# Kernel optimization log

Hardware: AMD Instinct MI355X
Metric: run time of the kernel (lower is better)

The kernel has to match this reference:

```python
import jax, jax.numpy as jnp
import numpy as np

D = 128  # embedding dim (hardcoded by nn.Linear(128*2, 1))


def setup_inputs() -> dict:
    key = jax.random.key(0)
    k1, k2, k3, k4 = jax.random.split(key, 4)
    B, T, N = 256, 64, 2048
    targetsentence_emb = jax.random.normal(k1, (B, T, D), dtype=jnp.float32)
    context_emb = jax.random.normal(k2, (B, N, D), dtype=jnp.float32)
    # Linear(2D -> 1): weight [1, 2D], bias [1]. Store as flat vectors.
    W = jax.random.normal(k3, (2 * D,), dtype=jnp.float32) * (1.0 / np.sqrt(2 * D))
    b = jax.random.normal(k4, (1,), dtype=jnp.float32) * 0.01
    return {"targetsentence_emb": targetsentence_emb, "context_emb": context_emb, "W": W, "b": b}


def reference(targetsentence_emb, context_emb, W, b):
    # Decompose concat+Linear: W = [Wt | Wc], both length D.
    Wt, Wc = W[:D], W[D:]
    T = targetsentence_emb.shape[1]
    # score[b, n] = sum_t (Wt . target[b,t] + Wc . ctx[b,n] + bias)
    #            = sum_t(Wt . target[b,t]) + T * (Wc . ctx[b,n] + bias)
    tgt_term = jnp.einsum('btd,d->b', targetsentence_emb, Wt)  # [B]
    ctx_term = jnp.einsum('bnd,d->bn', context_emb, Wc)        # [B, N]
    scores = tgt_term[:, None] + T * (ctx_term + b[0])         # [B, N]
    attention = jax.nn.softmax(scores, axis=1)                 # softmax over context dim
    # einsum 'bnm,bnk->bnk' with m=1 is elementwise broadcast scaling
    return attention[:, :, None] * context_emb                 # [B, N, D]
```

## Files before the change

### kernel.cpp

```cpp
#include <hip/hip_runtime.h>


#define B_DIM 256
#define N_DIM 2048
#define D_DIM 128
#define DVEC  (D_DIM / 4)
#define NTHR  1024
#define T_SCALE 64.0f

typedef float f4v __attribute__((ext_vector_type(4)));

__global__ __launch_bounds__(NTHR)
void k_fused(const float* __restrict__ ctx, const float* __restrict__ W,
             float* __restrict__ out) {
    const int tid  = threadIdx.x;
    const int wave = tid >> 6;
    const int lane = tid & 63;
    const int sub  = lane & 31;
    const int half = lane >> 5;
    const int b    = blockIdx.x;

    __shared__ float sm[N_DIM];
    __shared__ float red[16];

    const size_t cbase = (size_t)b * ((size_t)N_DIM * DVEC);
    const f4v* __restrict__ c4 = (const f4v*)ctx + cbase;
    f4v*       __restrict__ o4 = (f4v*)out + cbase;

    const f4v wc = ((const f4v*)(W + D_DIM))[sub];

    #pragma unroll 4
    for (int it = 0; it < N_DIM / 32; ++it) {
        const int n = it * 32 + wave * 2 + half;
        const f4v v = c4[(size_t)n * DVEC + sub];
        float p = v.x * wc.x + v.y * wc.y + v.z * wc.z + v.w * wc.w;
        #pragma unroll
        for (int m = 1; m < 32; m <<= 1) p += __shfl_xor(p, m, 64);
        if (sub == 0) sm[n] = T_SCALE * p;
    }
    __syncthreads();

    const float a0 = sm[tid];
    const float a1 = sm[tid + NTHR];
    float mx = fmaxf(a0, a1);
    #pragma unroll
    for (int m = 1; m < 64; m <<= 1) mx = fmaxf(mx, __shfl_xor(mx, m, 64));
    if (lane == 0) red[wave] = mx;
    __syncthreads();
    float gmax = red[0];
    #pragma unroll
    for (int i = 1; i < 16; ++i) gmax = fmaxf(gmax, red[i]);

    const float e0 = __expf(a0 - gmax);
    const float e1 = __expf(a1 - gmax);
    float s = e0 + e1;
    #pragma unroll
    for (int m = 1; m < 64; m <<= 1) s += __shfl_xor(s, m, 64);
    __syncthreads();
    if (lane == 0) red[wave] = s;
    __syncthreads();
    float tot = red[0];
    #pragma unroll
    for (int i = 1; i < 16; ++i) tot += red[i];
    const float inv = 1.0f / tot;

    sm[tid]        = e0 * inv;
    sm[tid + NTHR] = e1 * inv;
    __syncthreads();

    #pragma unroll 4
    for (int i = 0; i < (N_DIM * DVEC) / NTHR; ++i) {
        const int f = i * NTHR + tid;
        const float w = sm[f >> 5];
        f4v v = __builtin_nontemporal_load(&c4[f]);
        v *= w;
        __builtin_nontemporal_store(v, &o4[f]);
    }
}

extern "C" void kernel_launch(void* const* d_in, const int* in_sizes, int n_in,
                              void* d_out, int out_size, void* d_ws, size_t ws_size,
                              hipStream_t stream) {
    (void)in_sizes; (void)n_in; (void)out_size; (void)d_ws; (void)ws_size;
    const float* ctx = (const float*)d_in[1];
    const float* W   = (const float*)d_in[2];
    float* out       = (float*)d_out;

    hipLaunchKernelGGL(k_fused, dim3(B_DIM), dim3(NTHR), 0, stream,
                       ctx, W, out);
}
```

Before: 473.6 us.

## Stage context tiles through padded LDS with register prefetch for score dot products

Replaces the shuffle-reduction score pass with a tiled scheme. Each tile of 64 context rows is loaded coalesced into padded shared memory, while the next tile is prefetched into registers. Each wave computes partial dot products over an 8-element slice of D, and the partials are summed across waves through shared memory. This removes the per-row butterfly shuffles, at the cost of two block barriers per tile and extra LDS traffic in a loop that is now serialized.

```diff
diff --git a/kernel.cpp b/kernel.cpp
--- a/kernel.cpp
+++ b/kernel.cpp
@@ -6,6 +6,9 @@
 #define D_DIM 128
 #define DVEC  (D_DIM / 4)
 #define NTHR  1024
+#define TILE  64
+#define NTILE (N_DIM / TILE)
+#define LSTR  132
 #define T_SCALE 64.0f
 
 typedef float f4v __attribute__((ext_vector_type(4)));
@@ -16,29 +19,60 @@
     const int tid  = threadIdx.x;
     const int wave = tid >> 6;
     const int lane = tid & 63;
-    const int sub  = lane & 31;
-    const int half = lane >> 5;
     const int b    = blockIdx.x;
 
+    __shared__ float tb[TILE * LSTR];
     __shared__ float sm[N_DIM];
+    __shared__ float ps[16 * TILE];
     __shared__ float red[16];
 
-    const size_t cbase = (size_t)b * ((size_t)N_DIM * DVEC);
-    const f4v* __restrict__ c4 = (const f4v*)ctx + cbase;
-    f4v*       __restrict__ o4 = (f4v*)out + cbase;
+    const f4v* __restrict__ c4 = (const f4v*)ctx + (size_t)b * N_DIM * DVEC;
+    f4v*       __restrict__ o4 = (f4v*)out + (size_t)b * N_DIM * DVEC;
 
-    const f4v wc = ((const f4v*)(W + D_DIM))[sub];
+    const f4v wc0 = ((const f4v*)(W + D_DIM))[wave * 2];
+    const f4v wc1 = ((const f4v*)(W + D_DIM))[wave * 2 + 1];
 
-    #pragma unroll 4
-    for (int it = 0; it < N_DIM / 32; ++it) {
-        const int n = it * 32 + wave * 2 + half;
-        const f4v v = c4[(size_t)n * DVEC + sub];
-        float p = v.x * wc.x + v.y * wc.y + v.z * wc.z + v.w * wc.w;
-        #pragma unroll
-        for (int m = 1; m < 32; m <<= 1) p += __shfl_xor(p, m, 64);
-        if (sub == 0) sm[n] = T_SCALE * p;
+    const int sr = tid >> 5;
+    const int sc = (tid & 31) * 4;
+
+    {
+        f4v r0 = c4[tid];
+        f4v r1 = c4[1024 + tid];
+        *(f4v*)&tb[sr * LSTR + sc]        = r0;
+        *(f4v*)&tb[(32 + sr) * LSTR + sc] = r1;
     }
     __syncthreads();
+
+    #pragma unroll 1
+    for (int t = 0; t < NTILE; ++t) {
+        f4v n0, n1;
+        if (t < NTILE - 1) {
+            const int gb = (t + 1) * (TILE * DVEC);
+            n0 = c4[gb + tid];
+            n1 = c4[gb + 1024 + tid];
+        }
+        __builtin_amdgcn_sched_barrier(0);
+
+        const float* rb = &tb[lane * LSTR + wave * 8];
+        const f4v a = *(const f4v*)rb;
+        const f4v c = *(const f4v*)(rb + 4);
+        const float p = a.x * wc0.x + a.y * wc0.y + a.z * wc0.z + a.w * wc0.w
+                      + c.x * wc1.x + c.y * wc1.y + c.z * wc1.z + c.w * wc1.w;
+        ps[wave * TILE + lane] = p;
+        __syncthreads();
+
+        if (tid < TILE) {
+            float s = 0.f;
+            #pragma unroll
+            for (int q = 0; q < 16; ++q) s += ps[q * TILE + tid];
+            sm[t * TILE + tid] = T_SCALE * s;
+        }
+        if (t < NTILE - 1) {
+            *(f4v*)&tb[sr * LSTR + sc]        = n0;
+            *(f4v*)&tb[(32 + sr) * LSTR + sc] = n1;
+        }
+        __syncthreads();
+    }
 
     const float a0 = sm[tid];
     const float a1 = sm[tid + NTHR];
```

Result: no change. 479.3 us (+1.2%).
